# Kernel optimization log

Hardware: AMD Instinct MI355X
Metric: run time of the kernel (lower is better)

## Reference

```python
import jax, jax.numpy as jnp
import numpy as np

B = 8192          # batch
LATENT = 32       # latent_dim
H = 64            # hidden_size
SEQ_LEN = 180
NUM_CLASSES = 6
IN = 2            # GRU input size (zeros) / output features


def setup_inputs() -> dict:
    key = jax.random.key(0)
    ks = jax.random.split(key, 12)
    s_fc = 1.0 / np.sqrt(LATENT + H)
    s_rnn = 1.0 / np.sqrt(H)
    return {
        "z": jax.random.normal(ks[0], (B, LATENT), dtype=jnp.float32),
        "labels": jax.random.randint(ks[1], (B,), 0, NUM_CLASSES),
        "embed_w": jax.random.normal(ks[2], (NUM_CLASSES, H), dtype=jnp.float32),
        "fc_w": jax.random.uniform(ks[3], (H, LATENT + H), jnp.float32, -s_fc, s_fc),
        "fc_b": jax.random.uniform(ks[4], (H,), jnp.float32, -s_fc, s_fc),
        "w_ih": jax.random.uniform(ks[5], (3 * H, IN), jnp.float32, -s_rnn, s_rnn),
        "w_hh": jax.random.uniform(ks[6], (3 * H, H), jnp.float32, -s_rnn, s_rnn),
        "b_ih": jax.random.uniform(ks[7], (3 * H,), jnp.float32, -s_rnn, s_rnn),
        "b_hh": jax.random.uniform(ks[8], (3 * H,), jnp.float32, -s_rnn, s_rnn),
        "out_w": jax.random.uniform(ks[9], (IN, H), jnp.float32, -s_rnn, s_rnn),
        "out_b": jax.random.uniform(ks[10], (IN,), jnp.float32, -s_rnn, s_rnn),
    }


def reference(z, labels, embed_w, fc_w, fc_b, w_ih, w_hh, b_ih, b_hh, out_w, out_b):
    # h0 = tanh(fc([z, embed(labels)]))  -> [B, H]
    cond = embed_w[labels]
    h0 = jnp.tanh(jnp.concatenate([z, cond], axis=1) @ fc_w.T + fc_b)

    # GRU input is all zeros, so the input-side gates are constant per step:
    # gi = x_t @ w_ih.T + b_ih = b_ih  (kept faithful to torch GRU math)
    i_r, i_z, i_n = jnp.split(b_ih, 3)

    def step(h, _):
        gh = h @ w_hh.T + b_hh                      # [B, 3H]
        h_r, h_z, h_n = jnp.split(gh, 3, axis=-1)
        r = jax.nn.sigmoid(i_r + h_r)
        zg = jax.nn.sigmoid(i_z + h_z)
        n = jnp.tanh(i_n + r * h_n)
        h_new = (1.0 - zg) * n + zg * h
        return h_new, h_new

    _, hs = jax.lax.scan(step, h0, None, length=SEQ_LEN)  # [S, B, H]
    # out linear: [B, S, 2]
    return jnp.einsum("sbh,oh->bso", hs, out_w) + out_b
```

## Files before the change

kernel.cpp:

```cpp
#include <hip/hip_runtime.h>

#define NB     8192
#define HDIM   64
#define SEQ    180
#define MT     16
#define SB     72
#define XSP    100

typedef __bf16 bf16x8 __attribute__((ext_vector_type(8)));
typedef __bf16 bf16x4 __attribute__((ext_vector_type(4)));
typedef float  f32x4  __attribute__((ext_vector_type(4)));

#define L2E 1.44269504088896340736f

__device__ __forceinline__ float tanh_f(float x) {
    float e = __builtin_amdgcn_exp2f((2.0f * L2E) * x);
    return 1.0f - 2.0f * __builtin_amdgcn_rcpf(1.0f + e);
}

#define MFMA __builtin_amdgcn_mfma_f32_16x16x32_bf16

#define BAR_LDS() asm volatile("s_waitcnt lgkmcnt(0)\n\ts_barrier" ::: "memory")

__global__ __launch_bounds__(256) void gru_all(
        const float* __restrict__ z, const int* __restrict__ labels,
        const float* __restrict__ embed_w, const float* __restrict__ fc_w,
        const float* __restrict__ fc_b, const float* __restrict__ w_hh,
        const float* __restrict__ b_ih, const float* __restrict__ b_hh,
        const float* __restrict__ out_w, const float* __restrict__ out_b,
        float* __restrict__ out) {
    __shared__ __align__(16) __bf16 hbuf[2][MT * SB];
    __shared__ __align__(16) float  xs[MT * XSP];

    const int t = threadIdx.x;
    const int w = t >> 6;
    const int l = t & 63;
    const int q = l >> 4;
    const int n16 = l & 15;
    const int jg = 16 * w + n16;
    const int jb = 16 * w + 4 * q;
    const int bbase = blockIdx.x * MT;

    for (int c = t; c < MT * 24; c += 256) {
        int m = c / 24, kk = (c % 24) * 4;
        f32x4 v;
        if (kk < 32) v = *(const f32x4*)(z + (size_t)(bbase + m) * 32 + kk);
        else         v = *(const f32x4*)(embed_w + labels[bbase + m] * 64 + (kk - 32));
        *(f32x4*)(xs + m * XSP + kk) = v;
    }

    bf16x8 whi[3][2];
#pragma unroll
    for (int g = 0; g < 3; ++g) {
        const float* pr = w_hh + (g * 64 + jg) * HDIM;
#pragma unroll
        for (int ks = 0; ks < 2; ++ks) {
            const float* p = pr + ks * 32 + q * 8;
            f32x4 va = *(const f32x4*)(p);
            f32x4 vb = *(const f32x4*)(p + 4);
#pragma unroll
            for (int j2 = 0; j2 < 4; ++j2) {
                whi[g][ks][j2]     = (__bf16)va[j2];
                whi[g][ks][4 + j2] = (__bf16)vb[j2];
            }
        }
    }

    bf16x8 obhi[2];
#pragma unroll
    for (int ks = 0; ks < 2; ++ks) {
        f32x4 va = {0.f, 0.f, 0.f, 0.f}, vb = {0.f, 0.f, 0.f, 0.f};
        if (n16 < 2) {
            va = *(const f32x4*)(out_w + n16 * 64 + ks * 32 + q * 8);
            vb = *(const f32x4*)(out_w + n16 * 64 + ks * 32 + q * 8 + 4);
        }
#pragma unroll
        for (int j2 = 0; j2 < 4; ++j2) {
            obhi[ks][j2]     = (__bf16)va[j2];
            obhi[ks][4 + j2] = (__bf16)vb[j2];
        }
    }
    const f32x4 obias = (q == 0) ? f32x4{out_b[0], out_b[1], 0.f, 0.f}
                                 : f32x4{0.f, 0.f, 0.f, 0.f};
    const f32x4 kZ = {0.f, 0.f, 0.f, 0.f};
    const f32x4 one4 = {1.f, 1.f, 1.f, 1.f};

    const bool ostorer = (q == 0) && ((n16 >> 2) == w);

    const f32x4 bihR = *(const f32x4*)(b_ih + jb);
    const f32x4 bhhR = *(const f32x4*)(b_hh + jb);
    const f32x4 bihZ = *(const f32x4*)(b_ih + 64 + jb);
    const f32x4 bhhZ = *(const f32x4*)(b_hh + 64 + jb);
    const f32x4 cR4 = (bihR + bhhR) * (-L2E);
    const f32x4 cZ4 = (bihZ + bhhZ) * (-L2E);
    const f32x4 bn4 = *(const f32x4*)(b_hh + 128 + jb);
    const f32x4 cN4 = (*(const f32x4*)(b_ih + 128 + jb)) * (2.0f * L2E);

    const int rdoff = n16 * SB + q * 8;
    const int wboff = n16 * SB + jb;
    float* opb = out + (size_t)(bbase + n16) * (SEQ * 2);

    __syncthreads();

    f32x4 hprev;
    {
        f32x4 a = *(const f32x4*)(fc_b + jb);
        for (int kc = 0; kc < 24; ++kc) {
            f32x4 xv = *(const f32x4*)(xs + n16 * XSP + kc * 4);
#pragma unroll
            for (int r = 0; r < 4; ++r) {
                f32x4 wv = *(const f32x4*)(fc_w + (size_t)(jb + r) * 96 + kc * 4);
                a[r] += wv[0] * xv[0] + wv[1] * xv[1] + wv[2] * xv[2] + wv[3] * xv[3];
            }
        }
        bf16x4 hp;
#pragma unroll
        for (int r = 0; r < 4; ++r) {
            hprev[r] = tanh_f(a[r]);
            hp[r] = (__bf16)hprev[r];
        }
        *(bf16x4*)(hbuf[0] + wboff) = hp;
    }
    __syncthreads();

    if ((blockIdx.x >> 8) & 1) __builtin_amdgcn_s_sleep(8);

    for (int u = 0; u < SEQ / 4; ++u) {
#pragma unroll
        for (int s = 0; s < 4; ++s) {
            const int p = s & 1;
            const __bf16* Hh = hbuf[p];
            __bf16* Nh = hbuf[1 - p];

            bf16x8 b0 = *(const bf16x8*)(Hh + rdoff);
            bf16x8 b1 = *(const bf16x8*)(Hh + rdoff + 32);

            f32x4 aR, aZ, aN;
            aR = MFMA(whi[0][0], b0, kZ, 0, 0, 0);
            aZ = MFMA(whi[1][0], b0, kZ, 0, 0, 0);
            aN = MFMA(whi[2][0], b0, kZ, 0, 0, 0);
            aR = MFMA(whi[0][1], b1, aR, 0, 0, 0);
            aZ = MFMA(whi[1][1], b1, aZ, 0, 0, 0);
            aN = MFMA(whi[2][1], b1, aN, 0, 0, 0);

            f32x4 tR = aR * (-L2E) + cR4;
            f32x4 tZ = aZ * (-L2E) + cZ4;
            f32x4 eR, eZ;
#pragma unroll
            for (int r = 0; r < 4; ++r) {
                eR[r] = __builtin_amdgcn_exp2f(tR[r]);
                eZ[r] = __builtin_amdgcn_exp2f(tZ[r]);
            }
            eR = eR + one4;
            eZ = eZ + one4;
            f32x4 rg, zg;
#pragma unroll
            for (int r = 0; r < 4; ++r) {
                rg[r] = __builtin_amdgcn_rcpf(eR[r]);
                zg[r] = __builtin_amdgcn_rcpf(eZ[r]);
            }
            f32x4 mm = aN + bn4;
            f32x4 tN = (rg * mm) * (2.0f * L2E) + cN4;
            f32x4 eN;
#pragma unroll
            for (int r = 0; r < 4; ++r) eN[r] = __builtin_amdgcn_exp2f(tN[r]);
            eN = eN + one4;
            f32x4 dd;
#pragma unroll
            for (int r = 0; r < 4; ++r) dd[r] = __builtin_amdgcn_rcpf(eN[r]);
            f32x4 ng = dd * (-2.0f) + one4;
            f32x4 hn = zg * (hprev - ng) + ng;
            hprev = hn;
            bf16x4 hp;
#pragma unroll
            for (int r = 0; r < 4; ++r) hp[r] = (__bf16)hn[r];
            *(bf16x4*)(Nh + wboff) = hp;

            {
                f32x4 o = obias;
                o = MFMA(obhi[0], b0, o, 0, 0, 0);
                o = MFMA(obhi[1], b1, o, 0, 0, 0);
                if ((u | s) != 0 && ostorer)
                    *(float2*)(opb + (8 * u + 2 * s - 2)) = make_float2(o[0], o[1]);
            }

            BAR_LDS();
        }
    }

    {
        const __bf16* Hh = hbuf[0];
        bf16x8 b0 = *(const bf16x8*)(Hh + rdoff);
        bf16x8 b1 = *(const bf16x8*)(Hh + rdoff + 32);
        f32x4 o = obias;
        o = MFMA(obhi[0], b0, o, 0, 0, 0);
        o = MFMA(obhi[1], b1, o, 0, 0, 0);
        if (ostorer)
            *(float2*)(opb + (SEQ - 1) * 2) = make_float2(o[0], o[1]);
    }
}

extern "C" void kernel_launch(void* const* d_in, const int* in_sizes, int n_in,
                              void* d_out, int out_size, void* d_ws, size_t ws_size,
                              hipStream_t stream) {
    (void)in_sizes; (void)n_in; (void)out_size; (void)d_ws; (void)ws_size;
    const float* z       = (const float*)d_in[0];
    const int*   labels  = (const int*)d_in[1];
    const float* embed_w = (const float*)d_in[2];
    const float* fc_w    = (const float*)d_in[3];
    const float* fc_b    = (const float*)d_in[4];
    const float* w_hh    = (const float*)d_in[6];
    const float* b_ih    = (const float*)d_in[7];
    const float* b_hh    = (const float*)d_in[8];
    const float* out_w   = (const float*)d_in[9];
    const float* out_b   = (const float*)d_in[10];
    float* out = (float*)d_out;

    gru_all<<<NB / MT, 256, 0, stream>>>(z, labels, embed_w, fc_w, fc_b,
                                         w_hh, b_ih, b_hh, out_w, out_b, out);
}
```

Measured before the change: 171.7 us.

## Merge z-gate and tanh reciprocals and defer output projection one step

Rewrites the GRU update so the z-gate sigmoid and the tanh of the candidate share a single reciprocal, computing h_new as one numerator times one reciprocal of a combined denominator. This removes two of the four reciprocals per element on the serial recurrence path. It also moves the output-projection MFMA to use the previous step's hidden-state registers at the start of the next step, so it can overlap with the gate MFMAs instead of sitting after the state write. The combined formula may lose some precision or overflow when the exponentials are large, and the deferred projection adds an epilogue store for the second-to-last step.

```diff
diff --git a/kernel.cpp b/kernel.cpp
--- a/kernel.cpp
+++ b/kernel.cpp
@@ -125,6 +125,8 @@
 
     if ((blockIdx.x >> 8) & 1) __builtin_amdgcn_s_sleep(8);
 
+    bf16x8 pb0 = {}, pb1 = {};
+
     for (int u = 0; u < SEQ / 4; ++u) {
 #pragma unroll
         for (int s = 0; s < 4; ++s) {
@@ -134,6 +136,14 @@
 
             bf16x8 b0 = *(const bf16x8*)(Hh + rdoff);
             bf16x8 b1 = *(const bf16x8*)(Hh + rdoff + 32);
+
+            {
+                f32x4 o = obias;
+                o = MFMA(obhi[0], pb0, o, 0, 0, 0);
+                o = MFMA(obhi[1], pb1, o, 0, 0, 0);
+                if ((u > 0 || s >= 2) && ostorer)
+                    *(float2*)(opb + (8 * u + 2 * s - 4)) = make_float2(o[0], o[1]);
+            }
 
             f32x4 aR, aZ, aN;
             aR = MFMA(whi[0][0], b0, kZ, 0, 0, 0);
@@ -151,52 +161,51 @@
                 eR[r] = __builtin_amdgcn_exp2f(tR[r]);
                 eZ[r] = __builtin_amdgcn_exp2f(tZ[r]);
             }
-            eR = eR + one4;
-            eZ = eZ + one4;
-            f32x4 rg, zg;
-#pragma unroll
-            for (int r = 0; r < 4; ++r) {
-                rg[r] = __builtin_amdgcn_rcpf(eR[r]);
-                zg[r] = __builtin_amdgcn_rcpf(eZ[r]);
-            }
+            f32x4 A = eR + one4;
+            f32x4 rg;
+#pragma unroll
+            for (int r = 0; r < 4; ++r) rg[r] = __builtin_amdgcn_rcpf(A[r]);
             f32x4 mm = aN + bn4;
             f32x4 tN = (rg * mm) * (2.0f * L2E) + cN4;
             f32x4 eN;
 #pragma unroll
             for (int r = 0; r < 4; ++r) eN[r] = __builtin_amdgcn_exp2f(tN[r]);
-            eN = eN + one4;
-            f32x4 dd;
-#pragma unroll
-            for (int r = 0; r < 4; ++r) dd[r] = __builtin_amdgcn_rcpf(eN[r]);
-            f32x4 ng = dd * (-2.0f) + one4;
-            f32x4 hn = zg * (hprev - ng) + ng;
+            f32x4 wz = eZ + one4;
+            f32x4 pz = eZ + hprev;
+            f32x4 qz = hprev - eZ;
+            f32x4 Nst = eN * pz + qz;
+            f32x4 Dst = eN * wz + wz;
+            f32x4 rD;
+#pragma unroll
+            for (int r = 0; r < 4; ++r) rD[r] = __builtin_amdgcn_rcpf(Dst[r]);
+            f32x4 hn = Nst * rD;
             hprev = hn;
             bf16x4 hp;
 #pragma unroll
             for (int r = 0; r < 4; ++r) hp[r] = (__bf16)hn[r];
             *(bf16x4*)(Nh + wboff) = hp;
 
-            {
-                f32x4 o = obias;
-                o = MFMA(obhi[0], b0, o, 0, 0, 0);
-                o = MFMA(obhi[1], b1, o, 0, 0, 0);
-                if ((u | s) != 0 && ostorer)
-                    *(float2*)(opb + (8 * u + 2 * s - 2)) = make_float2(o[0], o[1]);
-            }
+            pb0 = b0; pb1 = b1;
 
             BAR_LDS();
         }
     }
 
     {
+        f32x4 o = obias;
+        o = MFMA(obhi[0], pb0, o, 0, 0, 0);
+        o = MFMA(obhi[1], pb1, o, 0, 0, 0);
+        if (ostorer)
+            *(float2*)(opb + (SEQ - 2) * 2) = make_float2(o[0], o[1]);
+
         const __bf16* Hh = hbuf[0];
         bf16x8 b0 = *(const bf16x8*)(Hh + rdoff);
         bf16x8 b1 = *(const bf16x8*)(Hh + rdoff + 32);
-        f32x4 o = obias;
-        o = MFMA(obhi[0], b0, o, 0, 0, 0);
-        o = MFMA(obhi[1], b1, o, 0, 0, 0);
+        f32x4 o2 = obias;
+        o2 = MFMA(obhi[0], b0, o2, 0, 0, 0);
+        o2 = MFMA(obhi[1], b1, o2, 0, 0, 0);
         if (ostorer)
-            *(float2*)(opb + (SEQ - 1) * 2) = make_float2(o[0], o[1]);
+            *(float2*)(opb + (SEQ - 1) * 2) = make_float2(o2[0], o2[1]);
     }
 }
 
```

Result: faster. 165.3 us (-3.7%).
